# Kernel optimization log

Hardware: AMD Instinct MI355X
Metric: run time of the kernel (lower is better)

Reference implementation:

```python
import jax, jax.numpy as jnp
import numpy as np
import math

INPUT_DIM = 1024
EMBED_DIM = 1024
NUM_HEADS = 16
HEAD_DIM = EMBED_DIM // NUM_HEADS


def setup_inputs() -> dict:
    key = jax.random.key(0)
    k_x, k_qkv, k_out_w, k_out_b = jax.random.split(key, 4)
    x = jax.random.normal(k_x, (1, 4096, INPUT_DIM), dtype=jnp.float32)
    # nn.Linear weights are [out, in]; kaiming-uniform-ish scale
    s1 = 1.0 / math.sqrt(INPUT_DIM)
    s2 = 1.0 / math.sqrt(EMBED_DIM)
    qkv_w = jax.random.uniform(k_qkv, (3 * EMBED_DIM, INPUT_DIM), jnp.float32, -s1, s1)
    out_w = jax.random.uniform(k_out_w, (EMBED_DIM, EMBED_DIM), jnp.float32, -s2, s2)
    out_b = jax.random.uniform(k_out_b, (EMBED_DIM,), jnp.float32, -s2, s2)
    return {"x": x, "qkv_w": qkv_w, "out_w": out_w, "out_b": out_b}


def reference(x, qkv_w, out_w, out_b):
    B, N, C = x.shape
    qkv = jnp.einsum('bnc,ec->bne', x, qkv_w)  # [B,N,3E]
    q = qkv[:, :, 0:EMBED_DIM].reshape(B, N, NUM_HEADS, HEAD_DIM)
    k = qkv[:, :, EMBED_DIM:2 * EMBED_DIM].reshape(B, N, NUM_HEADS, HEAD_DIM)
    v = qkv[:, :, 2 * EMBED_DIM:].reshape(B, N, NUM_HEADS, HEAD_DIM)
    scores = jnp.einsum('bihd,bjhd->bhij', q, k) / jnp.sqrt(jnp.float32(HEAD_DIM))
    attn = jax.nn.softmax(scores, axis=-1)  # [B,H,N,N]
    out = jnp.einsum('bhik,bkhd->bhid', attn, v)
    out = out.transpose(0, 2, 1, 3).reshape(B, N, EMBED_DIM)
    return jnp.einsum('bne,fe->bnf', out, out_w) + out_b
```

## Files before the change

kernel.cpp:

```cpp
#include <hip/hip_runtime.h>
#include <hip/hip_bf16.h>

typedef __bf16 bf16;
typedef bf16 bf16x8 __attribute__((ext_vector_type(8)));
typedef bf16 bf16x4 __attribute__((ext_vector_type(4)));
typedef float f32x4 __attribute__((ext_vector_type(4)));

#define MFMA16(a, b, c) __builtin_amdgcn_mfma_f32_16x16x32_bf16(a, b, c, 0, 0, 0)

__device__ __forceinline__ void g2l16(const bf16* g, bf16* l) {
  __builtin_amdgcn_global_load_lds(
      (__attribute__((address_space(1))) void*)(void*)g,
      (__attribute__((address_space(3))) void*)l,
      16, 0, 0);
}

__device__ __forceinline__ int sniff_inblock(const void* x, int tid) {
  __shared__ int sf;
  if (tid < 64) {
    unsigned short v = ((const unsigned short*)x)[tid];
    int e = (v >> 7) & 0xFF;
    int sane = (e == 0) || (e >= 112 && e <= 142);
    unsigned long long m = __ballot(sane);
    if (tid == 0) sf = (__popcll(m) >= 56) ? 1 : 0;
  }
  __syncthreads();
  return sf;
}

__device__ __forceinline__ void conv8(const void* in, bf16* out, long i, int f) {
  if (f) {
    ((bf16x8*)out)[i] = ((const bf16x8*)in)[i];
  } else {
    const float4* p = (const float4*)in;
    float4 a = p[i * 2], b = p[i * 2 + 1];
    bf16x8 v;
    v[0] = (bf16)a.x; v[1] = (bf16)a.y; v[2] = (bf16)a.z; v[3] = (bf16)a.w;
    v[4] = (bf16)b.x; v[5] = (bf16)b.y; v[6] = (bf16)b.z; v[7] = (bf16)b.w;
    ((bf16x8*)out)[i] = v;
  }
}

__global__ void convert2_to_bf16(const void* __restrict__ a, bf16* __restrict__ oa,
                                 long na8, const void* __restrict__ b,
                                 bf16* __restrict__ ob, long nb8,
                                 const void* __restrict__ x) {
  const int f = sniff_inblock(x, threadIdx.x);
  long i = (long)blockIdx.x * 256 + threadIdx.x;
  if (i < na8) conv8(a, oa, i, f);
  else if (i - na8 < nb8) conv8(b, ob, i - na8, f);
}

__global__ __launch_bounds__(256) void gemm_qkv(
    const bf16* __restrict__ A, const bf16* __restrict__ B,
    bf16* __restrict__ qB, bf16* __restrict__ kP, bf16* __restrict__ vP) {
  __shared__ __align__(16) bf16 As[128 * 32];
  __shared__ __align__(16) bf16 Bs[128 * 32];

  const int tid  = threadIdx.x;
  const int lane = tid & 63;
  const int wave = tid >> 6;
  const int wm   = wave >> 1, wn = wave & 1;
  const int l15  = lane & 15, quad = lane >> 4;
  const long m0 = (long)blockIdx.x * 128;
  const long n0 = (long)blockIdx.y * 128;
  const int  K  = 1024;

  const bf16* Ab = A + m0 * K;
  const bf16* Bb = B + n0 * K;
  const int rowA = tid & 127;
  const int dc   = tid >> 7;

  f32x4 acc[4][4] = {};

  for (int k0 = 0; k0 < K; k0 += 32) {
    g2l16(Ab + (long)rowA * K + k0 + dc * 8,       As + tid * 8);
    g2l16(Ab + (long)rowA * K + k0 + (dc + 2) * 8, As + (tid + 256) * 8);
    g2l16(Bb + (long)rowA * K + k0 + dc * 8,       Bs + tid * 8);
    g2l16(Bb + (long)rowA * K + k0 + (dc + 2) * 8, Bs + (tid + 256) * 8);
    __syncthreads();

    bf16x8 af[4], bfr[4];
#pragma unroll
    for (int t = 0; t < 4; t++) {
      af[t]  = *(const bf16x8*)(As + (quad * 128 + wm * 64 + t * 16 + l15) * 8);
      bfr[t] = *(const bf16x8*)(Bs + (quad * 128 + wn * 64 + t * 16 + l15) * 8);
    }
#pragma unroll
    for (int tm = 0; tm < 4; tm++)
#pragma unroll
      for (int tn = 0; tn < 4; tn++)
        acc[tm][tn] = MFMA16(af[tm], bfr[tn], acc[tm][tn]);
    __syncthreads();
  }

  const long rb = m0 + wm * 64;
  const long cb = n0 + wn * 64;
  const int third = (int)(n0 >> 10);
  const float QSC = 0.125f * 1.44269504088896f;

#pragma unroll
  for (int tm = 0; tm < 4; tm++) {
#pragma unroll
    for (int tn = 0; tn < 4; tn++) {
      const long r0 = rb + tm * 16 + quad * 4;
      const long c  = cb + tn * 16 + l15;
      if (third == 0) {
#pragma unroll
        for (int r = 0; r < 4; r++)
          qB[(r0 + r) * 1024 + c] = (bf16)(acc[tm][tn][r] * QSC);
      } else if (third == 1) {
        const int ep = (int)c - 1024;
        const int h = ep >> 6, d = ep & 63;
        const int n0r = (int)r0;
        const int kt = n0r >> 6;
        const int kh = (n0r >> 5) & 1;
        const int t_ = (n0r >> 2) & 1;
        const int mq = (n0r >> 3) & 3;
        const long base = ((long)h * 64 + kt) * 4096 +
                          (((d >> 3) * 64) + kh * 32 + t_ * 16 + mq * 4) * 8 +
                          (d & 7);
#pragma unroll
        for (int r = 0; r < 4; r++)
          kP[base + r * 8] = (bf16)acc[tm][tn][r];
      } else {
        const int ep = (int)c - 2048;
        const int h = ep >> 6, d = ep & 63;
        const int n0r = (int)r0;
        const int kt = n0r >> 6;
        const int kh = (n0r >> 5) & 1;
        const int kq = (n0r >> 3) & 3;
        bf16x4 v;
#pragma unroll
        for (int r = 0; r < 4; r++) v[r] = (bf16)acc[tm][tn][r];
        *(bf16x4*)(vP + ((long)h * 64 + kt) * 4096 +
                   (kh * 256 + kq * 64 + d) * 8 + (quad & 1) * 4) = v;
      }
    }
  }
}

template <bool BIAS, bool DYNOUT>
__global__ __launch_bounds__(256) void gemm_bt(
    const bf16* __restrict__ A, const bf16* __restrict__ B,
    void* __restrict__ Cv, const bf16* __restrict__ bias,
    int M, int Nn, int K, const void* __restrict__ xs) {
  __shared__ __align__(16) bf16 As[128 * 32];
  __shared__ __align__(16) bf16 Bs[64 * 32];

  const int tid  = threadIdx.x;
  const int obf = DYNOUT ? sniff_inblock(xs, tid) : 1;

  const int lane = tid & 63;
  const int wave = tid >> 6;
  const int wm   = wave >> 1, wn = wave & 1;
  const int l15  = lane & 15, quad = lane >> 4;
  const long m0 = (long)blockIdx.x * 128;
  const long n0 = (long)blockIdx.y * 64;

  const bf16* Ab = A + m0 * K;
  const bf16* Bb = B + n0 * K;
  const int rowA = tid & 127;
  const int dc   = tid >> 7;
  const int rowB = tid & 63;
  const int kcB  = tid >> 6;

  f32x4 acc[4][2] = {};

  for (int k0 = 0; k0 < K; k0 += 32) {
    g2l16(Ab + (long)rowA * K + k0 + dc * 8,       As + tid * 8);
    g2l16(Ab + (long)rowA * K + k0 + (dc + 2) * 8, As + (tid + 256) * 8);
    g2l16(Bb + (long)rowB * K + k0 + kcB * 8,      Bs + tid * 8);
    __syncthreads();

    bf16x8 af[4], bfr[2];
#pragma unroll
    for (int t = 0; t < 4; t++)
      af[t]  = *(const bf16x8*)(As + (quad * 128 + wm * 64 + t * 16 + l15) * 8);
#pragma unroll
    for (int t = 0; t < 2; t++)
      bfr[t] = *(const bf16x8*)(Bs + (quad * 64 + wn * 32 + t * 16 + l15) * 8);
#pragma unroll
    for (int tm = 0; tm < 4; tm++)
#pragma unroll
      for (int tn = 0; tn < 2; tn++)
        acc[tm][tn] = MFMA16(af[tm], bfr[tn], acc[tm][tn]);
    __syncthreads();
  }

  const long rb = m0 + wm * 64;
  const long cb = n0 + wn * 32;
#pragma unroll
  for (int tm = 0; tm < 4; tm++) {
#pragma unroll
    for (int tn = 0; tn < 2; tn++) {
      const long r0 = rb + tm * 16 + quad * 4;
      const long c  = cb + tn * 16 + l15;
      const float bv = BIAS ? (float)bias[c] : 0.0f;
#pragma unroll
      for (int r = 0; r < 4; r++) {
        const float val = acc[tm][tn][r] + bv;
        const long idx = (r0 + r) * Nn + c;
        if (DYNOUT && !obf) ((float*)Cv)[idx] = val;
        else                ((bf16*)Cv)[idx]  = (bf16)val;
      }
    }
  }
}

__device__ __forceinline__ void attn_tile(
    int kt, const bf16* kb, const bf16* vb, int quad, int koff, int voff,
    const bf16x8 (&qf)[4][2], const bf16x8 (&kcur)[2][2], bf16x8 (&knxt)[2][2],
    const bf16x8& onesf, f32x4 (&oa)[4][4], f32x4 (&la)[4]) {
  bf16x8 vf[4];
  const bf16* vt = vb + (long)kt * 4096;
#pragma unroll
  for (int dt = 0; dt < 4; dt++)
    vf[dt] = *(const bf16x8*)(vt + dt * 128 + voff);

  f32x4 s[4][2];
#pragma unroll
  for (int t = 0; t < 2; t++) {
    __builtin_amdgcn_s_setprio(1);
#pragma unroll
    for (int g = 0; g < 4; g++) {
      f32x4 z = {};
      z = MFMA16(kcur[t][0], qf[g][0], z);
      z = MFMA16(kcur[t][1], qf[g][1], z);
      s[g][t] = z;
    }
    __builtin_amdgcn_s_setprio(0);
  }

  const bf16* kn = kb + (long)(kt + 1) * 4096;
#pragma unroll
  for (int t = 0; t < 2; t++)
#pragma unroll
    for (int j = 0; j < 2; j++)
      knxt[t][j] = *(const bf16x8*)(kn + (j * 4 + quad) * 512 + t * 128 + koff);

  bf16x8 pf[4];
#pragma unroll
  for (int g = 0; g < 4; g++) {
    union { bf16x8 v; __hip_bfloat162 h2[4]; } u;
#pragma unroll
    for (int idx = 0; idx < 4; idx++) {
      const int t = idx >> 1, rr = (idx & 1) * 2;
      float p0 = __builtin_amdgcn_exp2f(s[g][t][rr]);
      float p1 = __builtin_amdgcn_exp2f(s[g][t][rr + 1]);
      u.h2[idx] = __float22bfloat162_rn(float2{p0, p1});
    }
    pf[g] = u.v;
  }

#pragma unroll
  for (int dt = 0; dt < 4; dt++) {
    __builtin_amdgcn_s_setprio(1);
#pragma unroll
    for (int g = 0; g < 4; g++) oa[g][dt] = MFMA16(vf[dt], pf[g], oa[g][dt]);
    __builtin_amdgcn_s_setprio(0);
  }
  __builtin_amdgcn_s_setprio(1);
#pragma unroll
  for (int g = 0; g < 4; g++) la[g] = MFMA16(onesf, pf[g], la[g]);
  __builtin_amdgcn_s_setprio(0);
}

__global__ __launch_bounds__(128, 2) void flash_attn(
    const bf16* __restrict__ qB, const bf16* __restrict__ kP,
    const bf16* __restrict__ vP, bf16* __restrict__ O) {
  __shared__ __align__(16) float red[4096];
  __shared__ float lred[256];

  const int tid = threadIdx.x;
  const int lane = tid & 63;
  const int kh = tid >> 6;
  const int l15 = lane & 15, quad = lane >> 4;
  const int bid = blockIdx.x;
  const int xcd = bid & 7, bi = bid >> 3;
  const int h  = xcd + 8 * (bi >> 6);
  const int qt = bi & 63;
  const int q0 = qt * 64;

  {
    const int slot = (bid >> 8) & 3;
    if (slot == 1)      __builtin_amdgcn_s_sleep(10);
    else if (slot == 2) __builtin_amdgcn_s_sleep(20);
    else if (slot == 3) __builtin_amdgcn_s_sleep(30);
  }

  bf16x8 qf[4][2];
#pragma unroll
  for (int g = 0; g < 4; g++) {
    const bf16* qrow = qB + (long)(q0 + g * 16 + l15) * 1024 + h * 64;
    qf[g][0] = *(const bf16x8*)(qrow + quad * 8);
    qf[g][1] = *(const bf16x8*)(qrow + 32 + quad * 8);
  }

  bf16x8 onesf;
#pragma unroll
  for (int j = 0; j < 8; j++) onesf[j] = (bf16)1.0f;

  f32x4 oa[4][4] = {};
  f32x4 la[4] = {};

  const bf16* kb = kP + (long)h * 64 * 4096;
  const bf16* vb = vP + (long)h * 64 * 4096;

  const int koff = (kh * 32 + l15) * 8;
  const int voff = (kh * 256 + quad * 64 + l15) * 8;

  bf16x8 kA[2][2], kB[2][2];
#pragma unroll
  for (int t = 0; t < 2; t++)
#pragma unroll
    for (int j = 0; j < 2; j++)
      kA[t][j] = *(const bf16x8*)(kb + (j * 4 + quad) * 512 + t * 128 + koff);

#pragma unroll 1
  for (int kt = 0; kt < 64; kt += 2) {
    attn_tile(kt,     kb, vb, quad, koff, voff, qf, kA, kB, onesf, oa, la);
    attn_tile(kt + 1, kb, vb, quad, koff, voff, qf, kB, kA, onesf, oa, la);
  }

  if (kh == 1) {
#pragma unroll
    for (int g = 0; g < 4; g++)
#pragma unroll
      for (int dt = 0; dt < 4; dt++)
        *(f32x4*)(red + (g * 4 + dt) * 256 + lane * 4) = oa[g][dt];
#pragma unroll
    for (int g = 0; g < 4; g++) lred[g * 64 + lane] = la[g][0];
  }
  __syncthreads();
  if (kh == 0) {
#pragma unroll
    for (int g = 0; g < 4; g++) {
#pragma unroll
      for (int dt = 0; dt < 4; dt++)
        oa[g][dt] += *(const f32x4*)(red + (g * 4 + dt) * 256 + lane * 4);
      const float l = la[g][0] + lred[g * 64 + lane];
      const float inv = 1.0f / l;
      bf16* orow = O + (long)(q0 + g * 16 + l15) * 1024 + h * 64;
#pragma unroll
      for (int dt = 0; dt < 4; dt++) {
        bf16x4 v;
#pragma unroll
        for (int r = 0; r < 4; r++) v[r] = (bf16)(oa[g][dt][r] * inv);
        *(bf16x4*)(orow + dt * 16 + quad * 4) = v;
      }
    }
  }
}

extern "C" void kernel_launch(void* const* d_in, const int* in_sizes, int n_in,
                              void* d_out, int out_size, void* d_ws, size_t ws_size,
                              hipStream_t stream) {
  const void* x     = d_in[0];
  const void* qkv_w = d_in[1];
  const void* out_w = d_in[2];
  const void* out_b = d_in[3];

  char* ws = (char*)d_ws;
  bf16* qB   = (bf16*)(ws);
  bf16* kP   = (bf16*)(ws + 8388608);
  bf16* vP   = (bf16*)(ws + 16777216);
  bf16* ob   = (bf16*)(ws + 25165824);
  bf16* qwb  = (bf16*)(ws + 33554432);
  bf16* xb   = ob;
  bf16* owb  = qB;
  bf16* obb  = qB + 1048576;

  convert2_to_bf16<<<3584, 256, 0, stream>>>(x, xb, 524288, qkv_w, qwb, 393216, x);

  gemm_qkv<<<dim3(32, 24), 256, 0, stream>>>(xb, qwb, qB, kP, vP);

  flash_attn<<<1024, 128, 0, stream>>>(qB, kP, vP, ob);

  convert2_to_bf16<<<513, 256, 0, stream>>>(out_w, owb, 131072, out_b, obb, 128, x);

  gemm_bt<true, true><<<dim3(32, 16), 256, 0, stream>>>(
      ob, owb, d_out, obb, 4096, 1024, 1024, x);
}
```

Before: 229.5 us.

## Triple-buffer LDS in QKV and output GEMMs with async prefetch pipeline

```diff
diff --git a/kernel.cpp b/kernel.cpp
--- a/kernel.cpp
+++ b/kernel.cpp
@@ -54,8 +54,8 @@
 __global__ __launch_bounds__(256) void gemm_qkv(
     const bf16* __restrict__ A, const bf16* __restrict__ B,
     bf16* __restrict__ qB, bf16* __restrict__ kP, bf16* __restrict__ vP) {
-  __shared__ __align__(16) bf16 As[128 * 32];
-  __shared__ __align__(16) bf16 Bs[128 * 32];
+  __shared__ __align__(16) bf16 As[3][128 * 32];
+  __shared__ __align__(16) bf16 Bs[3][128 * 32];
 
   const int tid  = threadIdx.x;
   const int lane = tid & 63;
@@ -73,26 +73,43 @@
 
   f32x4 acc[4][4] = {};
 
-  for (int k0 = 0; k0 < K; k0 += 32) {
-    g2l16(Ab + (long)rowA * K + k0 + dc * 8,       As + tid * 8);
-    g2l16(Ab + (long)rowA * K + k0 + (dc + 2) * 8, As + (tid + 256) * 8);
-    g2l16(Bb + (long)rowA * K + k0 + dc * 8,       Bs + tid * 8);
-    g2l16(Bb + (long)rowA * K + k0 + (dc + 2) * 8, Bs + (tid + 256) * 8);
-    __syncthreads();
-
+#define QKV_STAGE(t, buf)                                                     \
+  {                                                                           \
+    const long kk = (long)(t) * 32;                                           \
+    g2l16(Ab + (long)rowA * K + kk + dc * 8,       As[buf] + tid * 8);        \
+    g2l16(Ab + (long)rowA * K + kk + (dc + 2) * 8, As[buf] + (tid + 256) * 8);\
+    g2l16(Bb + (long)rowA * K + kk + dc * 8,       Bs[buf] + tid * 8);        \
+    g2l16(Bb + (long)rowA * K + kk + (dc + 2) * 8, Bs[buf] + (tid + 256) * 8);\
+  }
+
+  QKV_STAGE(0, 0)
+  QKV_STAGE(1, 1)
+
+  for (int i = 0; i < 32; ++i) {
+    if (i < 31) asm volatile("s_waitcnt vmcnt(4)" ::: "memory");
+    else        asm volatile("s_waitcnt vmcnt(0)" ::: "memory");
+    __builtin_amdgcn_s_barrier();
+
+    if (i + 2 < 32) {
+      const int nb = (i + 2) % 3;
+      QKV_STAGE(i + 2, nb)
+    }
+
+    const bf16* Ac = As[i % 3];
+    const bf16* Bc = Bs[i % 3];
     bf16x8 af[4], bfr[4];
 #pragma unroll
     for (int t = 0; t < 4; t++) {
-      af[t]  = *(const bf16x8*)(As + (quad * 128 + wm * 64 + t * 16 + l15) * 8);
-      bfr[t] = *(const bf16x8*)(Bs + (quad * 128 + wn * 64 + t * 16 + l15) * 8);
+      af[t]  = *(const bf16x8*)(Ac + (quad * 128 + wm * 64 + t * 16 + l15) * 8);
+      bfr[t] = *(const bf16x8*)(Bc + (quad * 128 + wn * 64 + t * 16 + l15) * 8);
     }
 #pragma unroll
     for (int tm = 0; tm < 4; tm++)
 #pragma unroll
       for (int tn = 0; tn < 4; tn++)
         acc[tm][tn] = MFMA16(af[tm], bfr[tn], acc[tm][tn]);
-    __syncthreads();
-  }
+  }
+#undef QKV_STAGE
 
   const long rb = m0 + wm * 64;
   const long cb = n0 + wn * 64;
@@ -145,8 +162,8 @@
     const bf16* __restrict__ A, const bf16* __restrict__ B,
     void* __restrict__ Cv, const bf16* __restrict__ bias,
     int M, int Nn, int K, const void* __restrict__ xs) {
-  __shared__ __align__(16) bf16 As[128 * 32];
-  __shared__ __align__(16) bf16 Bs[64 * 32];
+  __shared__ __align__(16) bf16 As[3][128 * 32];
+  __shared__ __align__(16) bf16 Bs[3][64 * 32];
 
   const int tid  = threadIdx.x;
   const int obf = DYNOUT ? sniff_inblock(xs, tid) : 1;
@@ -167,26 +184,43 @@
 
   f32x4 acc[4][2] = {};
 
-  for (int k0 = 0; k0 < K; k0 += 32) {
-    g2l16(Ab + (long)rowA * K + k0 + dc * 8,       As + tid * 8);
-    g2l16(Ab + (long)rowA * K + k0 + (dc + 2) * 8, As + (tid + 256) * 8);
-    g2l16(Bb + (long)rowB * K + k0 + kcB * 8,      Bs + tid * 8);
-    __syncthreads();
-
+#define BT_STAGE(t, buf)                                                      \
+  {                                                                           \
+    const long kk = (long)(t) * 32;                                           \
+    g2l16(Ab + (long)rowA * K + kk + dc * 8,       As[buf] + tid * 8);        \
+    g2l16(Ab + (long)rowA * K + kk + (dc + 2) * 8, As[buf] + (tid + 256) * 8);\
+    g2l16(Bb + (long)rowB * K + kk + kcB * 8,      Bs[buf] + tid * 8);        \
+  }
+
+  BT_STAGE(0, 0)
+  BT_STAGE(1, 1)
+
+  for (int i = 0; i < 32; ++i) {
+    if (i < 31) asm volatile("s_waitcnt vmcnt(3)" ::: "memory");
+    else        asm volatile("s_waitcnt vmcnt(0)" ::: "memory");
+    __builtin_amdgcn_s_barrier();
+
+    if (i + 2 < 32) {
+      const int nb = (i + 2) % 3;
+      BT_STAGE(i + 2, nb)
+    }
+
+    const bf16* Ac = As[i % 3];
+    const bf16* Bc = Bs[i % 3];
     bf16x8 af[4], bfr[2];
 #pragma unroll
     for (int t = 0; t < 4; t++)
-      af[t]  = *(const bf16x8*)(As + (quad * 128 + wm * 64 + t * 16 + l15) * 8);
+      af[t]  = *(const bf16x8*)(Ac + (quad * 128 + wm * 64 + t * 16 + l15) * 8);
 #pragma unroll
     for (int t = 0; t < 2; t++)
-      bfr[t] = *(const bf16x8*)(Bs + (quad * 64 + wn * 32 + t * 16 + l15) * 8);
+      bfr[t] = *(const bf16x8*)(Bc + (quad * 64 + wn * 32 + t * 16 + l15) * 8);
 #pragma unroll
     for (int tm = 0; tm < 4; tm++)
 #pragma unroll
       for (int tn = 0; tn < 2; tn++)
         acc[tm][tn] = MFMA16(af[tm], bfr[tn], acc[tm][tn]);
-    __syncthreads();
-  }
+  }
+#undef BT_STAGE
 
   const long rb = m0 + wm * 64;
   const long cb = n0 + wn * 32;
```

New measurement: 227.7 us. No clear change (-0.8%).
